# Kernel optimization log

Measured on AMD Instinct MI355X. Metric: run time of the kernel, lower is better.

## Reference

```python
import jax, jax.numpy as jnp
from jax import lax
import numpy as np

B, CIN, COUT, H, W, K = 4, 64, 64, 128, 128, 3
FACTOR = 2.0  # ivcf, tile != first-layer override path -> factor = ivcf
DN = ('NCHW', 'OIHW', 'NCHW')


def cimu_conv2d(x, weight, bias, factor):
    """Bit-serial int8 conv emulation: 8 bit-plane convs, per-plane clamp/round."""
    xq = jnp.clip(x, -128, 127).astype(jnp.int8).astype(jnp.uint8)  # two's complement bits
    shifts = jnp.arange(8, dtype=jnp.uint8).reshape(8, 1, 1, 1, 1)
    bits = ((xq[None] >> shifts) & jnp.uint8(1)).astype(jnp.float32)  # (8,B,C,Hp,Wp)
    P, b, c, hp, wp = bits.shape
    y = lax.conv_general_dilated(bits.reshape(P * b, c, hp, wp), weight,
                                 window_strides=(1, 1), padding='VALID',
                                 dimension_numbers=DN)  # (8B, Cout, Ho, Wo)
    y = y.reshape(P, b, y.shape[1], y.shape[2], y.shape[3])
    y = jnp.clip(jnp.round(y / factor), -128, 127)
    y = jnp.round(jnp.round(y * factor))
    plane_w = jnp.array([1., 2., 4., 8., 16., 32., 64., -128.], dtype=jnp.float32)
    y = jnp.einsum('pbchw,p->bchw', y, plane_w)
    return y + bias.reshape(1, -1, 1, 1)


def setup_inputs() -> dict:
    key = jax.random.key(0)
    ks = jax.random.split(key, 8)
    ri = lambda k, shape, lo, hi: (jax.random.randint(k, shape, lo, hi)).astype(jnp.float32)
    return {
        'cast_in':   ri(ks[0], (B, CIN, H, W), -128, 128),
        'merge_in':  ri(ks[1], (B, COUT, H, W), -128, 128),
        'gather_in': ri(ks[2], (B, COUT, H, W), -128, 128),
        'conv_weight': ri(ks[3], (COUT, CIN, K, K), -3, 4),
        'conv_bias':   ri(ks[4], (COUT,), -8, 8),
        'ctrans_i': ri(ks[5], (COUT,), 1, 4),            # per-channel integer multiplier
        'ctrans_s': jnp.full((COUT,), -1.0, jnp.float32),  # per-channel shift exponent
        'strans_i': jnp.float32(3.0),
        'strans_s': jnp.float32(-2.0),
        'atrans_i': jnp.float32(1.0),
        'atrans_s': jnp.float32(0.0),
    }


def reference(cast_in, merge_in, gather_in, conv_weight, conv_bias,
              ctrans_i, ctrans_s, strans_i, strans_s, atrans_i, atrans_s):
    # conv_pads = [1,1,1,1] (left,right,top,bottom on last two dims)
    x = jnp.pad(cast_in, ((0, 0), (0, 0), (1, 1), (1, 1)))
    x = cimu_conv2d(x, conv_weight, conv_bias, FACTOR)
    # merge add
    x = x + merge_in
    # merge-node quantize (hardtrans): mult = ctrans_i / 2^{-ctrans_s}
    cmult = (ctrans_i / (2.0 ** (-ctrans_s))).reshape(1, -1, 1, 1)
    x = jnp.clip(jnp.round(x * cmult), -128, 127)
    # gather add + quantize
    x = x + gather_in
    smult = strans_i / (2.0 ** (-strans_s))
    x = jnp.clip(jnp.round(x * smult), -128, 127)
    # Relu + quantize
    x = jax.nn.relu(x)
    amult = atrans_i / (2.0 ** (-atrans_s))
    x = jnp.clip(jnp.round(x * amult), -128, 127)
    # pool_pads = [0,0,0,0] (no-op), MaxPool 2x2 stride 2
    x = lax.reduce_window(x, -jnp.inf, lax.max, (1, 1, 2, 2), (1, 1, 2, 2), 'VALID')
    return x
```

## Files before the change

### kernel.cpp

```cpp
#include <hip/hip_runtime.h>
#include <cstdint>


typedef int i32x4  __attribute__((ext_vector_type(4)));
typedef int i32x16 __attribute__((ext_vector_type(16)));

#define XB_OFF   0u
#define XB_BYTES 4326400u
#define MG_OFF   (XB_OFF + XB_BYTES)
#define MG_BYTES 4194304u
#define GT_OFF   (MG_OFF + MG_BYTES)
#define WPK_OFF  (GT_OFF + MG_BYTES)
#define WPK_BYTES 36864u

__global__ __launch_bounds__(256) void k_stage(const float* __restrict__ s_cast,
                                               const float* __restrict__ s_mg,
                                               const float* __restrict__ s_gt,
                                               const float* __restrict__ wsrc,
                                               uint8_t* __restrict__ ws) {
  const int blk = blockIdx.x, t = threadIdx.x;
  if (blk >= 1680) {
    const int hb = blk - 1680;
    const int b = hb >> 1, r = (hb & 1) ? 129 : 0;
    uint8_t* base = ws + XB_OFF + ((size_t)(b * 130 + r) * 130) * 64;
    const uint4 z = {0, 0, 0, 0};
#pragma unroll
    for (int i = 0; i < 3; ++i) {
      const int s = i * 256 + t;
      if (s < 520) *(uint4*)(base + (size_t)s * 16) = z;
    }
    return;
  }
  if (blk >= 1536) {
    const int idx = (blk - 1536) * 256 + t;
    const int i = idx & 15, l = (idx >> 4) & 63, gg = (idx >> 10) & 1,
              c = idx >> 11;
    const int k = c * 32 + (l >> 5) * 16 + i;
    const int tap = k >> 6, ci = k & 63;
    const int kh = tap / 3, kw = tap % 3;
    const int cco = gg * 32 + (l & 31);
    const float wv = wsrc[((cco * 64 + ci) * 3 + kh) * 3 + kw];
    ((int8_t*)(ws + WPK_OFF))[idx] = (int8_t)(int)wv;
    return;
  }
  const int which = blk >> 9, rem = blk & 511;
  const float* src = which == 0 ? s_cast : (which == 1 ? s_mg : s_gt);
  uint8_t* dst = which == 0 ? (ws + XB_OFF)
                            : (which == 1 ? (ws + MG_OFF) : (ws + GT_OFF));
  const int b = rem >> 7, h = rem & 127;
  __shared__ uint8_t lds[128 * 68];
  const float* s0 = src + ((size_t)(b * 64) * 128 + h) * 128;
#pragma unroll
  for (int ci0 = 0; ci0 < 64; ci0 += 2) {
    const int ci = ci0 + (t >> 7), w = t & 127;
    const float v = s0[ci * 16384 + w];
    lds[w * 68 + ci] = (uint8_t)((int)v & 0xFF);
  }
  __syncthreads();
  if (which == 0) {
    uint8_t* row = dst + (((size_t)b * 130 + h + 1) * 130) * 64;
#pragma unroll
    for (int j = 0; j < 8; ++j) {
      const int f = j * 256 + t;
      const int w = f >> 4, ci4 = f & 15;
      const uint32_t val = *(const uint32_t*)&lds[w * 68 + ci4 * 4];
      *(uint32_t*)(row + 64 + (size_t)f * 4) = val;
    }
    if (t < 8) {
      const int col = (t < 4) ? 0 : 129, seg = t & 3;
      const uint4 z = {0, 0, 0, 0};
      *(uint4*)(row + (size_t)col * 64 + seg * 16) = z;
    }
  } else {
    uint8_t* d0 = dst + ((size_t)(b * 128 + h) * 128) * 64;
#pragma unroll
    for (int j = 0; j < 8; ++j) {
      const int f = j * 256 + t;
      const int w = f >> 4, ci4 = f & 15;
      const uint32_t val = *(const uint32_t*)&lds[w * 68 + ci4 * 4];
      *(uint32_t*)(d0 + (size_t)f * 4) = val;
    }
  }
}

__global__ __launch_bounds__(256, 4) void k_main(
    const unsigned char* __restrict__ xb, const signed char* __restrict__ mg,
    const signed char* __restrict__ gt, const int8_t* __restrict__ wpk,
    const float* __restrict__ bias, const float* __restrict__ cti,
    const float* __restrict__ cts, const float* __restrict__ sti,
    const float* __restrict__ sts, const float* __restrict__ ati,
    const float* __restrict__ ats, float* __restrict__ outp) {
  const int tid = threadIdx.x, lane = tid & 63, wvid = tid >> 6;
  const int g = wvid & 1;
  const int wog = wvid >> 1;
  const int blk = blockIdx.x;
  const int wq = blk & 3, ho = (blk >> 2) & 63, b = blk >> 8;
  const int h = ho * 2, w0 = wq * 32;

  __shared__ uint4 ldsx4[640];
  __shared__ float po_lds[16 * 64];
  uint8_t* ldsx = (uint8_t*)ldsx4;

  {
    const unsigned char* xrow = xb + ((size_t)(b * 130 + h) * 130 + w0) * 64;
#pragma unroll
    for (int i = 0; i < 3; ++i) {
      const int s = i * 256 + tid;
      if (s < 640) {
        const int row = s / 160, rm = s - row * 160;
        const int col = rm >> 2, ci16 = rm & 3;
        const int gcol = col < 34 ? col : 33;
        const uint4 v =
            *(const uint4*)(xrow + ((size_t)row * 130 + gcol) * 64 + ci16 * 16);
        *(uint4*)(ldsx + (row * 40 + col) * 64 + ci16 * 16) = v;
      }
    }
  }

  i32x4 Bf[18];
#pragma unroll
  for (int c = 0; c < 18; ++c)
    Bf[c] = *(const i32x4*)(wpk + ((size_t)(c * 2 + g) * 64 + lane) * 16);

  const int pix = (lane & 31) >> 3;
  const int plane = lane & 7;
  const int khalf = lane >> 5;
  const int dh = pix >> 1, dw = pix & 1;
  const uint8_t* lbase0 = ldsx + (dh * 40 + dw) * 64 + khalf * 16;

  const int co = g * 32 + (lane & 31);
  const float bs = bias[co];
  const float cm = ldexpf(cti[co], (int)cts[co]);
  const float sm = ldexpf(sti[0], (int)sts[0]);
  const float am = ldexpf(ati[0], (int)ats[0]);
  float pwl[4];
  pwl[0] = khalf ? 16.f : 1.f;
  pwl[1] = khalf ? 32.f : 2.f;
  pwl[2] = khalf ? 64.f : 4.f;
  pwl[3] = khalf ? -128.f : 8.f;

  __syncthreads();

  for (int q = 0; q < 8; ++q) {
    const int wol = wog * 8 + q;
    const int w = (wq * 16 + wol) * 2;
    const uint8_t* lb = lbase0 + wol * 128;

    int mgv[4], gtv[4];
#pragma unroll
    for (int px = 0; px < 4; ++px) {
      const size_t moff =
          ((size_t)((b * 128 + h + (px >> 1)) * 128 + w + (px & 1))) * 64 + co;
      mgv[px] = mg[moff];
      gtv[px] = gt[moff];
    }

    i32x16 acc = {};
#pragma unroll
    for (int c = 0; c < 18; ++c) {
      const int tap = c >> 1;
      const int kh = tap / 3, kw = tap % 3;
      const uint4 vv =
          *(const uint4*)(lb + kh * 2560 + kw * 64 + (c & 1) * 32);
      i32x4 av;
      av[0] = (int)((vv.x >> plane) & 0x01010101u);
      av[1] = (int)((vv.y >> plane) & 0x01010101u);
      av[2] = (int)((vv.z >> plane) & 0x01010101u);
      av[3] = (int)((vv.w >> plane) & 0x01010101u);
      acc = __builtin_amdgcn_mfma_i32_32x32x32_i8(av, Bf[c], acc, 0, 0, 0);
    }

    float psum[4];
#pragma unroll
    for (int px = 0; px < 4; ++px) {
      float s = 0.f;
#pragma unroll
      for (int j = 0; j < 4; ++j) {
        const float y = (float)acc[px * 4 + j];
        const float qq = fminf(fmaxf(rintf(y * 0.5f), -128.f), 127.f);
        s = fmaf(pwl[j], 2.f * qq, s);
      }
      psum[px] = s;
    }
#pragma unroll
    for (int px = 0; px < 4; ++px)
      psum[px] += __shfl_xor(psum[px], 32);

    float po = -3.0e38f;
#pragma unroll
    for (int px = 0; px < 4; ++px) {
      const float x1 = psum[px] + bs + (float)mgv[px];
      const float x2 = fminf(fmaxf(rintf(x1 * cm), -128.f), 127.f);
      const float x3 = x2 + (float)gtv[px];
      const float x4 = fminf(fmaxf(rintf(x3 * sm), -128.f), 127.f);
      const float x5 = fmaxf(x4, 0.f);
      const float x6 = fminf(fmaxf(rintf(x5 * am), -128.f), 127.f);
      po = fmaxf(po, x6);
    }
    if (lane < 32) po_lds[wol * 64 + co] = po;
  }

  __syncthreads();
  {
    const int tco = tid >> 2, seg = tid & 3;
    float4 v;
    v.x = po_lds[(seg * 4 + 0) * 64 + tco];
    v.y = po_lds[(seg * 4 + 1) * 64 + tco];
    v.z = po_lds[(seg * 4 + 2) * 64 + tco];
    v.w = po_lds[(seg * 4 + 3) * 64 + tco];
    float* dst = outp + (((size_t)(b * 64 + tco)) * 64 + ho) * 64 + wq * 16 + seg * 4;
    *(float4*)dst = v;
  }
}

extern "C" void kernel_launch(void* const* d_in, const int* in_sizes, int n_in,
                              void* d_out, int out_size, void* d_ws, size_t ws_size,
                              hipStream_t stream) {
  const float* cast_in = (const float*)d_in[0];
  const float* merge_in = (const float*)d_in[1];
  const float* gather_in = (const float*)d_in[2];
  const float* conv_w = (const float*)d_in[3];
  const float* conv_b = (const float*)d_in[4];
  const float* cti = (const float*)d_in[5];
  const float* cts = (const float*)d_in[6];
  const float* sti = (const float*)d_in[7];
  const float* sts = (const float*)d_in[8];
  const float* ati = (const float*)d_in[9];
  const float* ats = (const float*)d_in[10];

  uint8_t* ws = (uint8_t*)d_ws;
  uint8_t* xb = ws + XB_OFF;
  int8_t* mg = (int8_t*)(ws + MG_OFF);
  int8_t* gt = (int8_t*)(ws + GT_OFF);
  int8_t* wpk = (int8_t*)(ws + WPK_OFF);

  k_stage<<<1688, 256, 0, stream>>>(cast_in, merge_in, gather_in, conv_w, ws);
  k_main<<<1024, 256, 0, stream>>>(xb, mg, gt, wpk, conv_b, cti, cts, sti, sts,
                                   ati, ats, (float*)d_out);
}
```

Before: 41.32 us.

## Compute both output-channel halves per wave, reusing bit-plane A fragments across two MFMAs

Each wave now holds all 36 weight fragments and runs two MFMA accumulators, one per 32-channel half, over 4 pooled outputs instead of 8. Each unpacked bit-plane A fragment is built once and fed to two MFMAs, halving the LDS reads and shift/mask work per MFMA. LDS loads are software-prefetched three steps ahead. The cost is much higher register pressure (36 B fragments plus two 16-wide accumulators), so launch bounds drop to 2 blocks per SIMD-group, which lowers occupancy.

```diff
diff --git a/kernel.cpp b/kernel.cpp
--- a/kernel.cpp
+++ b/kernel.cpp
@@ -83,16 +83,14 @@
   }
 }
 
-__global__ __launch_bounds__(256, 4) void k_main(
+__global__ __launch_bounds__(256, 2) void k_main(
     const unsigned char* __restrict__ xb, const signed char* __restrict__ mg,
     const signed char* __restrict__ gt, const int8_t* __restrict__ wpk,
     const float* __restrict__ bias, const float* __restrict__ cti,
     const float* __restrict__ cts, const float* __restrict__ sti,
     const float* __restrict__ sts, const float* __restrict__ ati,
     const float* __restrict__ ats, float* __restrict__ outp) {
-  const int tid = threadIdx.x, lane = tid & 63, wvid = tid >> 6;
-  const int g = wvid & 1;
-  const int wog = wvid >> 1;
+  const int tid = threadIdx.x, lane = tid & 63, wv = tid >> 6;
   const int blk = blockIdx.x;
   const int wq = blk & 3, ho = (blk >> 2) & 63, b = blk >> 8;
   const int h = ho * 2, w0 = wq * 32;
@@ -117,10 +115,10 @@
     }
   }
 
-  i32x4 Bf[18];
-#pragma unroll
-  for (int c = 0; c < 18; ++c)
-    Bf[c] = *(const i32x4*)(wpk + ((size_t)(c * 2 + g) * 64 + lane) * 16);
+  i32x4 Bf[36];
+#pragma unroll
+  for (int cg = 0; cg < 36; ++cg)
+    Bf[cg] = *(const i32x4*)(wpk + ((size_t)cg * 64 + lane) * 16);
 
   const int pix = (lane & 31) >> 3;
   const int plane = lane & 7;
@@ -128,9 +126,10 @@
   const int dh = pix >> 1, dw = pix & 1;
   const uint8_t* lbase0 = ldsx + (dh * 40 + dw) * 64 + khalf * 16;
 
-  const int co = g * 32 + (lane & 31);
-  const float bs = bias[co];
-  const float cm = ldexpf(cti[co], (int)cts[co]);
+  const int col = lane & 31;
+  const float bs0 = bias[col], bs1 = bias[col + 32];
+  const float cm0 = ldexpf(cti[col], (int)cts[col]);
+  const float cm1 = ldexpf(cti[col + 32], (int)cts[col + 32]);
   const float sm = ldexpf(sti[0], (int)sts[0]);
   const float am = ldexpf(ati[0], (int)ats[0]);
   float pwl[4];
@@ -141,63 +140,84 @@
 
   __syncthreads();
 
-  for (int q = 0; q < 8; ++q) {
-    const int wol = wog * 8 + q;
+  for (int q = 0; q < 4; ++q) {
+    const int wol = wv * 4 + q;
     const int w = (wq * 16 + wol) * 2;
     const uint8_t* lb = lbase0 + wol * 128;
 
-    int mgv[4], gtv[4];
+    int mgv[8], gtv[8];
 #pragma unroll
     for (int px = 0; px < 4; ++px) {
       const size_t moff =
-          ((size_t)((b * 128 + h + (px >> 1)) * 128 + w + (px & 1))) * 64 + co;
+          ((size_t)((b * 128 + h + (px >> 1)) * 128 + w + (px & 1))) * 64 + col;
       mgv[px] = mg[moff];
       gtv[px] = gt[moff];
-    }
-
-    i32x16 acc = {};
+      mgv[4 + px] = mg[moff + 32];
+      gtv[4 + px] = gt[moff + 32];
+    }
+
+#define XOFF(c) ((((c) >> 1) / 3) * 2560 + (((c) >> 1) % 3) * 64 + ((c)&1) * 32)
+    uint4 p0 = *(const uint4*)(lb + XOFF(0));
+    uint4 p1 = *(const uint4*)(lb + XOFF(1));
+    uint4 p2 = *(const uint4*)(lb + XOFF(2));
+    i32x16 a0 = {}, a1 = {};
 #pragma unroll
     for (int c = 0; c < 18; ++c) {
-      const int tap = c >> 1;
-      const int kh = tap / 3, kw = tap % 3;
-      const uint4 vv =
-          *(const uint4*)(lb + kh * 2560 + kw * 64 + (c & 1) * 32);
+      uint4 cur;
+      if (c % 3 == 0) cur = p0;
+      else if (c % 3 == 1) cur = p1;
+      else cur = p2;
+      if (c + 3 < 18) {
+        const uint4 nv = *(const uint4*)(lb + XOFF(c + 3));
+        if (c % 3 == 0) p0 = nv;
+        else if (c % 3 == 1) p1 = nv;
+        else p2 = nv;
+      }
       i32x4 av;
-      av[0] = (int)((vv.x >> plane) & 0x01010101u);
-      av[1] = (int)((vv.y >> plane) & 0x01010101u);
-      av[2] = (int)((vv.z >> plane) & 0x01010101u);
-      av[3] = (int)((vv.w >> plane) & 0x01010101u);
-      acc = __builtin_amdgcn_mfma_i32_32x32x32_i8(av, Bf[c], acc, 0, 0, 0);
-    }
-
-    float psum[4];
-#pragma unroll
-    for (int px = 0; px < 4; ++px) {
-      float s = 0.f;
-#pragma unroll
-      for (int j = 0; j < 4; ++j) {
-        const float y = (float)acc[px * 4 + j];
-        const float qq = fminf(fmaxf(rintf(y * 0.5f), -128.f), 127.f);
-        s = fmaf(pwl[j], 2.f * qq, s);
-      }
-      psum[px] = s;
-    }
-#pragma unroll
-    for (int px = 0; px < 4; ++px)
-      psum[px] += __shfl_xor(psum[px], 32);
-
-    float po = -3.0e38f;
-#pragma unroll
-    for (int px = 0; px < 4; ++px) {
-      const float x1 = psum[px] + bs + (float)mgv[px];
-      const float x2 = fminf(fmaxf(rintf(x1 * cm), -128.f), 127.f);
-      const float x3 = x2 + (float)gtv[px];
-      const float x4 = fminf(fmaxf(rintf(x3 * sm), -128.f), 127.f);
-      const float x5 = fmaxf(x4, 0.f);
-      const float x6 = fminf(fmaxf(rintf(x5 * am), -128.f), 127.f);
-      po = fmaxf(po, x6);
-    }
-    if (lane < 32) po_lds[wol * 64 + co] = po;
+      av[0] = (int)((cur.x >> plane) & 0x01010101u);
+      av[1] = (int)((cur.y >> plane) & 0x01010101u);
+      av[2] = (int)((cur.z >> plane) & 0x01010101u);
+      av[3] = (int)((cur.w >> plane) & 0x01010101u);
+      a0 = __builtin_amdgcn_mfma_i32_32x32x32_i8(av, Bf[c * 2 + 0], a0, 0, 0, 0);
+      a1 = __builtin_amdgcn_mfma_i32_32x32x32_i8(av, Bf[c * 2 + 1], a1, 0, 0, 0);
+    }
+#undef XOFF
+
+#pragma unroll
+    for (int gg = 0; gg < 2; ++gg) {
+      const i32x16& acc = gg ? a1 : a0;
+      const float bs = gg ? bs1 : bs0;
+      const float cm = gg ? cm1 : cm0;
+      float psum[4];
+#pragma unroll
+      for (int px = 0; px < 4; ++px) {
+        float s = 0.f;
+#pragma unroll
+        for (int j = 0; j < 4; ++j) {
+          const float y = (float)acc[px * 4 + j];
+          const float qq = fminf(fmaxf(rintf(y * 0.5f), -128.f), 127.f);
+          s = fmaf(pwl[j], 2.f * qq, s);
+        }
+        psum[px] = s;
+      }
+#pragma unroll
+      for (int px = 0; px < 4; ++px)
+        psum[px] += __shfl_xor(psum[px], 32);
+
+      float po = -3.0e38f;
+#pragma unroll
+      for (int px = 0; px < 4; ++px) {
+        const float x1 = psum[px] + bs + (float)mgv[gg * 4 + px];
+        const float x2 = fminf(fmaxf(rintf(x1 * cm), -128.f), 127.f);
+        const float x3 = x2 + (float)gtv[gg * 4 + px];
+        const float x4 = fminf(fmaxf(rintf(x3 * sm), -128.f), 127.f);
+        const float x5 = fmaxf(x4, 0.f);
+        const float x6 = fminf(fmaxf(rintf(x5 * am), -128.f), 127.f);
+        po = fmaxf(po, x6);
+      }
+      if (lane < 32)
+        po_lds[wol * 64 + gg * 32 + col] = po;
+    }
   }
 
   __syncthreads();
```

After: 40.51 us. 1.02x faster.
